# Kernel tuning notes

Measured on AMD Instinct MI355X. Metric: run time of the kernel, lower is better.

The kernel has to match this reference:

```python
import jax, jax.numpy as jnp
import numpy as np

B, N, C = 8, 8192, 64
NPOINT, RADIUS, NSAMPLE = 2048, 0.2, 32


def setup_inputs() -> dict:
    key = jax.random.key(0)
    k1, k2 = jax.random.split(key)
    xyz = jax.random.uniform(k1, (B, N, 3), dtype=jnp.float32)      # unit-cube cloud
    points = jax.random.normal(k2, (B, N, C), dtype=jnp.float32)    # per-point features
    return {"xyz": xyz, "points": points}


def farthest_point_sample(xyz, npoint):
    """Iterative FPS. xyz: (B, N, 3) -> idx: (B, npoint) int32. Starts at index 0."""
    b, n, _ = xyz.shape

    def step(carry, _):
        dist, far = carry                                   # (B,N), (B,)
        centroid = jnp.take_along_axis(xyz, far[:, None, None], axis=1)  # (B,1,3)
        d = jnp.sum((xyz - centroid) ** 2, axis=-1)          # (B,N)
        dist = jnp.minimum(dist, d)
        new_far = jnp.argmax(dist, axis=-1).astype(jnp.int32)
        return (dist, new_far), far

    init = (jnp.full((b, n), jnp.inf, dtype=xyz.dtype), jnp.zeros((b,), jnp.int32))
    _, idx = jax.lax.scan(step, init, None, length=npoint)   # (npoint, B)
    return idx.T


def query_ball_point(radius, nsample, xyz, new_xyz):
    """For each query, first `nsample` point indices within radius (original order),
    padded with the first in-ball index (PointNet++ semantics)."""
    n = xyz.shape[1]
    # (B, M, N) pairwise squared distances
    dist2 = jnp.sum((new_xyz[:, :, None, :] - xyz[:, None, :, :]) ** 2, axis=-1)
    cand = jnp.where(dist2 < radius * radius, jnp.arange(n, dtype=jnp.int32), n)
    cand = jnp.sort(cand, axis=-1)[..., :nsample]            # first nsample in order
    first = cand[..., :1]                                    # seed itself is always in-ball
    return jnp.where(cand == n, first, cand)                 # (B, M, nsample)


def _gather(p, i):
    return p[i]


group = jax.vmap(_gather)  # (B,N,D), (B,...) -> (B,...,D)


def reference(xyz, points):
    fps_idx = farthest_point_sample(xyz, NPOINT)             # (B, npoint)
    new_xyz = group(xyz, fps_idx)                            # (B, npoint, 3)
    idx = query_ball_point(RADIUS, NSAMPLE, xyz, new_xyz)    # (B, npoint, nsample)
    grouped_xyz = group(xyz, idx) - new_xyz[:, :, None, :]   # recenter on seed
    grouped_points = group(points, idx)                      # (B, npoint, nsample, C)
    new_points = jnp.concatenate([grouped_xyz, grouped_points], axis=-1)
    return new_xyz, new_points
```

## Files before the change

### kernel.cpp

```cpp
#include <hip/hip_runtime.h>
#include <cstdint>

#define N_PTS   8192
#define N_BATCH 8
#define NPOINT  2048
#define NSAMPLE 32
#define C_FEAT  64
#define R2      0.04f
#define FPS_T   1024
#define CH      (N_PTS / FPS_T)
#define NBINS   512
#define NWAVE   (FPS_T / 64)

static __device__ __forceinline__ uint32_t spread3(uint32_t v) {
  return (v & 1u) | ((v & 2u) << 2) | ((v & 4u) << 4);
}

static __device__ __forceinline__ uint32_t cell_of(float x, float y, float z) {
  int ix = (int)(x * 8.0f); ix = ix < 0 ? 0 : (ix > 7 ? 7 : ix);
  int iy = (int)(y * 8.0f); iy = iy < 0 ? 0 : (iy > 7 ? 7 : iy);
  int iz = (int)(z * 8.0f); iz = iz < 0 ? 0 : (iz > 7 ? 7 : iz);
  return spread3((uint32_t)ix) | (spread3((uint32_t)iy) << 1) | (spread3((uint32_t)iz) << 2);
}

#define DPP_MAXD(v, CTRL) do {                                                          \
  uint64_t u_ = __builtin_bit_cast(uint64_t, v);                                        \
  int lo_ = __builtin_amdgcn_update_dpp(0, (int)(uint32_t)u_,         CTRL, 0xF, 0xF, true); \
  int hi_ = __builtin_amdgcn_update_dpp(0, (int)(uint32_t)(u_ >> 32), CTRL, 0xF, 0xF, true); \
  double p_ = __builtin_bit_cast(double, ((uint64_t)(uint32_t)hi_ << 32) | (uint64_t)(uint32_t)lo_); \
  v = __builtin_fmax(v, p_);                                                            \
} while (0)

__global__ __launch_bounds__(FPS_T) void fps_kernel(const float* __restrict__ xyz,
                                                    float* __restrict__ new_xyz) {
  __shared__ float sx[N_PTS], sy[N_PTS], sz[N_PTS];
  __shared__ int perm[N_PTS];
  __shared__ uint32_t bins[NBINS];
  __shared__ double pkey[2][NWAVE];
  float* cent = (float*)perm;

  const int b = blockIdx.x;
  const int t = threadIdx.x;
  const int lane = t & 63;
  const int w = t >> 6;
  const float* xb = xyz + (size_t)b * N_PTS * 3;

  for (int e = t; e < N_PTS * 3; e += FPS_T) {
    float v = xb[e];
    int p = e / 3, c = e - 3 * p;
    if (c == 0) sx[p] = v;
    else if (c == 1) sy[p] = v;
    else sz[p] = v;
  }
  if (t < NBINS) bins[t] = 0;
  __syncthreads();

#pragma unroll
  for (int k = 0; k < CH; ++k) {
    int p = k * FPS_T + t;
    atomicAdd(&bins[cell_of(sx[p], sy[p], sz[p])], 1u);
  }
  __syncthreads();

  if (t < 64) {
    uint32_t v[8], e[8], run = 0;
#pragma unroll
    for (int j = 0; j < 8; ++j) v[j] = bins[t * 8 + j];
#pragma unroll
    for (int j = 0; j < 8; ++j) { e[j] = run; run += v[j]; }
    uint32_t inc = run;
#pragma unroll
    for (int off = 1; off < 64; off <<= 1) {
      uint32_t o = __shfl_up(inc, off, 64);
      if (t >= off) inc += o;
    }
    uint32_t base = inc - run;
#pragma unroll
    for (int j = 0; j < 8; ++j) bins[t * 8 + j] = base + e[j];
  }
  __syncthreads();

#pragma unroll
  for (int k = 0; k < CH; ++k) {
    int p = k * FPS_T + t;
    uint32_t pos = atomicAdd(&bins[cell_of(sx[p], sy[p], sz[p])], 1u);
    perm[pos] = p;
  }
  __syncthreads();

  float rx[CH], ry[CH], rz[CH], dist[CH];
  uint32_t ridx[CH];
#pragma unroll
  for (int j = 0; j < CH; ++j) {
    int p = perm[CH * t + j];
    ridx[j] = (uint32_t)p;
    rx[j] = sx[p]; ry[j] = sy[p]; rz[j] = sz[p];
    dist[j] = __builtin_inff();
  }
  float bnx = rx[0], bxx = rx[0], bny = ry[0], bxy = ry[0], bnz = rz[0], bxz = rz[0];
#pragma unroll
  for (int j = 1; j < CH; ++j) {
    bnx = fminf(bnx, rx[j]); bxx = fmaxf(bxx, rx[j]);
    bny = fminf(bny, ry[j]); bxy = fmaxf(bxy, ry[j]);
    bnz = fminf(bnz, rz[j]); bxz = fmaxf(bxz, rz[j]);
  }
  __syncthreads();

  float cmax = __builtin_inff();
  uint32_t cidx = 0;
  double wkey = 0.0;
  int far = 0;

  for (int it = 0; it < NPOINT; ++it) {
    float cx = sx[far], cy = sy[far], cz = sz[far];
    if (t == 0) {
      cent[it * 3 + 0] = cx;
      cent[it * 3 + 1] = cy;
      cent[it * 3 + 2] = cz;
    }

    float gx = fmaxf(fmaxf(bnx - cx, cx - bxx), 0.0f);
    float gy = fmaxf(fmaxf(bny - cy, cy - bxy), 0.0f);
    float gz = fmaxf(fmaxf(bnz - cz, cz - bxz), 0.0f);
    float lb = gx * gx + gy * gy + gz * gz;

    bool act = !(lb * 0.99999f >= cmax);
    uint64_t am = __ballot(act);
    if (am != 0) {
      if (act) {
        {
#pragma clang fp contract(off)
#pragma unroll
          for (int j = 0; j < CH; ++j) {
            float dx = rx[j] - cx;
            float a = dx * dx;
            float dy = ry[j] - cy;
            a = a + dy * dy;
            float dz = rz[j] - cz;
            a = a + dz * dz;
            dist[j] = fminf(dist[j], a);
          }
        }
        float m0 = fmaxf(dist[0], dist[1]), m1 = fmaxf(dist[2], dist[3]);
        float m2 = fmaxf(dist[4], dist[5]), m3 = fmaxf(dist[6], dist[7]);
        cmax = fmaxf(fmaxf(m0, m1), fmaxf(m2, m3));
        uint32_t mi = 0xFFFFFFFFu;
#pragma unroll
        for (int j = 0; j < CH; ++j) {
          uint32_t cand = ridx[j] < mi ? ridx[j] : mi;
          mi = (dist[j] == cmax) ? cand : mi;
        }
        cidx = mi;
      }
      double key = __builtin_bit_cast(double,
          ((uint64_t)__builtin_bit_cast(uint32_t, cmax) << 32) |
          (uint64_t)(0xFFFFFFFFu - cidx));
      DPP_MAXD(key, 0x111);
      DPP_MAXD(key, 0x112);
      DPP_MAXD(key, 0x114);
      DPP_MAXD(key, 0x118);
      DPP_MAXD(key, 0x142);
      DPP_MAXD(key, 0x143);
      wkey = key;
    }
    if (lane == 63) pkey[it & 1][w] = wkey;
    __syncthreads();

    double g = pkey[it & 1][lane & 15];
    DPP_MAXD(g, 0x111);
    DPP_MAXD(g, 0x112);
    DPP_MAXD(g, 0x114);
    DPP_MAXD(g, 0x118);
    uint64_t gu = __builtin_bit_cast(uint64_t, g);
    uint32_t glo = (uint32_t)__builtin_amdgcn_readlane((int)(uint32_t)gu, 15);
    far = (int)(0xFFFFFFFFu - glo);
  }

  __syncthreads();
  float* ob = new_xyz + (size_t)b * NPOINT * 3;
  for (int e = t; e < NPOINT * 3; e += FPS_T) ob[e] = cent[e];
}

__global__ __launch_bounds__(256) void ball_group_kernel(const float* __restrict__ xyz,
                                                         const float* __restrict__ points,
                                                         const float* __restrict__ new_xyz,
                                                         float* __restrict__ out_np) {
  __shared__ int list[4][NSAMPLE];
  const int wslot = threadIdx.x >> 6;
  const int lane = threadIdx.x & 63;
  const int qg = blockIdx.x * 4 + wslot;
  const int b = qg >> 11;

  const float* xb = xyz + (size_t)b * N_PTS * 3;
  const float* nq = new_xyz + (size_t)qg * 3;
  const float cqx = nq[0], cqy = nq[1], cqz = nq[2];

  int K = 0;
  {
#pragma clang fp contract(off)
    for (int c = 0; c < N_PTS / 64; ++c) {
      const int pt = c * 64 + lane;
      const float* p = xb + pt * 3;
      float dx = cqx - p[0];
      float dy = cqy - p[1];
      float dz = cqz - p[2];
      float d2 = dx * dx;
      d2 = d2 + dy * dy;
      d2 = d2 + dz * dz;
      bool in = d2 < R2;
      unsigned long long mask = __ballot(in);
      if (in) {
        int rank = __builtin_amdgcn_mbcnt_hi((uint32_t)(mask >> 32),
                     __builtin_amdgcn_mbcnt_lo((uint32_t)mask, 0));
        int s = K + rank;
        if (s < NSAMPLE) list[wslot][s] = pt;
      }
      K += (int)__popcll(mask);
      if (K >= NSAMPLE) break;
    }
  }
  __builtin_amdgcn_wave_barrier();
  int Kc = K < NSAMPLE ? K : NSAMPLE;
  int first = list[wslot][0];
  if (lane >= Kc && lane < NSAMPLE) list[wslot][lane] = first;
  __builtin_amdgcn_wave_barrier();

  const float* pb = points + (size_t)b * N_PTS * C_FEAT;
  float* oq = out_np + (size_t)qg * (NSAMPLE * 67);
  for (int r = 0; r < 34; ++r) {
    int tt = r * 64 + lane;
    if (tt < NSAMPLE * 67) {
      int s = tt / 67;
      int f = tt - s * 67;
      int idx = list[wslot][s];
      float val;
      if (f < 3) {
        float cf = (f == 0) ? cqx : ((f == 1) ? cqy : cqz);
        val = xb[idx * 3 + f] - cf;
      } else {
        val = pb[(size_t)idx * C_FEAT + (f - 3)];
      }
      oq[tt] = val;
    }
  }
}

extern "C" void kernel_launch(void* const* d_in, const int* in_sizes, int n_in,
                              void* d_out, int out_size, void* d_ws, size_t ws_size,
                              hipStream_t stream) {
  const float* xyz = (const float*)d_in[0];
  const float* points = (const float*)d_in[1];
  float* out = (float*)d_out;
  float* new_xyz = out;
  float* new_points = out + (size_t)N_BATCH * NPOINT * 3;

  fps_kernel<<<N_BATCH, FPS_T, 0, stream>>>(xyz, new_xyz);
  ball_group_kernel<<<(N_BATCH * NPOINT) / 4, 256, 0, stream>>>(xyz, points, new_xyz, new_points);
}
```

Before: 1.374 ms.

## Halve FPS block size, store coordinates interleaved, use fmed3 for box bound

Reduces the FPS block from 1024 to 512 threads, so each thread holds 16 points in registers and the cross-wave reduction covers 8 waves instead of 16. Shared coordinates move from three separate SoA arrays to one interleaved array, which turns the load into a straight copy. The box lower-bound distance now uses fmed3. Fewer waves make each per-iteration barrier and reduction cheaper, but each thread does twice the distance work per iteration and uses more registers.

```diff
diff --git a/kernel.cpp b/kernel.cpp
--- a/kernel.cpp
+++ b/kernel.cpp
@@ -7,7 +7,7 @@
 #define NSAMPLE 32
 #define C_FEAT  64
 #define R2      0.04f
-#define FPS_T   1024
+#define FPS_T   512
 #define CH      (N_PTS / FPS_T)
 #define NBINS   512
 #define NWAVE   (FPS_T / 64)
@@ -33,7 +33,7 @@
 
 __global__ __launch_bounds__(FPS_T) void fps_kernel(const float* __restrict__ xyz,
                                                     float* __restrict__ new_xyz) {
-  __shared__ float sx[N_PTS], sy[N_PTS], sz[N_PTS];
+  __shared__ float scrd[N_PTS * 3];
   __shared__ int perm[N_PTS];
   __shared__ uint32_t bins[NBINS];
   __shared__ double pkey[2][NWAVE];
@@ -45,20 +45,14 @@
   const int w = t >> 6;
   const float* xb = xyz + (size_t)b * N_PTS * 3;
 
-  for (int e = t; e < N_PTS * 3; e += FPS_T) {
-    float v = xb[e];
-    int p = e / 3, c = e - 3 * p;
-    if (c == 0) sx[p] = v;
-    else if (c == 1) sy[p] = v;
-    else sz[p] = v;
-  }
-  if (t < NBINS) bins[t] = 0;
+  for (int e = t; e < N_PTS * 3; e += FPS_T) scrd[e] = xb[e];
+  bins[t] = 0;
   __syncthreads();
 
 #pragma unroll
   for (int k = 0; k < CH; ++k) {
     int p = k * FPS_T + t;
-    atomicAdd(&bins[cell_of(sx[p], sy[p], sz[p])], 1u);
+    atomicAdd(&bins[cell_of(scrd[3 * p], scrd[3 * p + 1], scrd[3 * p + 2])], 1u);
   }
   __syncthreads();
 
@@ -83,7 +77,7 @@
 #pragma unroll
   for (int k = 0; k < CH; ++k) {
     int p = k * FPS_T + t;
-    uint32_t pos = atomicAdd(&bins[cell_of(sx[p], sy[p], sz[p])], 1u);
+    uint32_t pos = atomicAdd(&bins[cell_of(scrd[3 * p], scrd[3 * p + 1], scrd[3 * p + 2])], 1u);
     perm[pos] = p;
   }
   __syncthreads();
@@ -94,7 +88,7 @@
   for (int j = 0; j < CH; ++j) {
     int p = perm[CH * t + j];
     ridx[j] = (uint32_t)p;
-    rx[j] = sx[p]; ry[j] = sy[p]; rz[j] = sz[p];
+    rx[j] = scrd[3 * p]; ry[j] = scrd[3 * p + 1]; rz[j] = scrd[3 * p + 2];
     dist[j] = __builtin_inff();
   }
   float bnx = rx[0], bxx = rx[0], bny = ry[0], bxy = ry[0], bnz = rz[0], bxz = rz[0];
@@ -112,16 +106,16 @@
   int far = 0;
 
   for (int it = 0; it < NPOINT; ++it) {
-    float cx = sx[far], cy = sy[far], cz = sz[far];
+    float cx = scrd[3 * far], cy = scrd[3 * far + 1], cz = scrd[3 * far + 2];
     if (t == 0) {
       cent[it * 3 + 0] = cx;
       cent[it * 3 + 1] = cy;
       cent[it * 3 + 2] = cz;
     }
 
-    float gx = fmaxf(fmaxf(bnx - cx, cx - bxx), 0.0f);
-    float gy = fmaxf(fmaxf(bny - cy, cy - bxy), 0.0f);
-    float gz = fmaxf(fmaxf(bnz - cz, cz - bxz), 0.0f);
+    float gx = cx - __builtin_amdgcn_fmed3f(cx, bnx, bxx);
+    float gy = cy - __builtin_amdgcn_fmed3f(cy, bny, bxy);
+    float gz = cz - __builtin_amdgcn_fmed3f(cz, bnz, bxz);
     float lb = gx * gx + gy * gy + gz * gz;
 
     bool act = !(lb * 0.99999f >= cmax);
@@ -141,9 +135,12 @@
             dist[j] = fminf(dist[j], a);
           }
         }
-        float m0 = fmaxf(dist[0], dist[1]), m1 = fmaxf(dist[2], dist[3]);
-        float m2 = fmaxf(dist[4], dist[5]), m3 = fmaxf(dist[6], dist[7]);
-        cmax = fmaxf(fmaxf(m0, m1), fmaxf(m2, m3));
+        float m0 = fmaxf(dist[0], dist[1]),  m1 = fmaxf(dist[2], dist[3]);
+        float m2 = fmaxf(dist[4], dist[5]),  m3 = fmaxf(dist[6], dist[7]);
+        float m4 = fmaxf(dist[8], dist[9]),  m5 = fmaxf(dist[10], dist[11]);
+        float m6 = fmaxf(dist[12], dist[13]), m7 = fmaxf(dist[14], dist[15]);
+        m0 = fmaxf(m0, m1); m2 = fmaxf(m2, m3); m4 = fmaxf(m4, m5); m6 = fmaxf(m6, m7);
+        cmax = fmaxf(fmaxf(m0, m2), fmaxf(m4, m6));
         uint32_t mi = 0xFFFFFFFFu;
 #pragma unroll
         for (int j = 0; j < CH; ++j) {
@@ -166,13 +163,12 @@
     if (lane == 63) pkey[it & 1][w] = wkey;
     __syncthreads();
 
-    double g = pkey[it & 1][lane & 15];
+    double g = pkey[it & 1][lane & 7];
     DPP_MAXD(g, 0x111);
     DPP_MAXD(g, 0x112);
     DPP_MAXD(g, 0x114);
-    DPP_MAXD(g, 0x118);
     uint64_t gu = __builtin_bit_cast(uint64_t, g);
-    uint32_t glo = (uint32_t)__builtin_amdgcn_readlane((int)(uint32_t)gu, 15);
+    uint32_t glo = (uint32_t)__builtin_amdgcn_readlane((int)(uint32_t)gu, 7);
     far = (int)(0xFFFFFFFFu - glo);
   }
 
```

Measured after the change: 2.002 ms. +45.7%, slower.
